# Kernel optimization log

Hardware: AMD Instinct MI355X
Metric: run time of the kernel (lower is better)

## Reference

```python
import jax, jax.numpy as jnp
import numpy as np

# --- fixed OpenCV filter kernels ---
# cv2.getGaussianKernel(3, 1): exp(-(i-1)^2/2), normalized -> [0.27407, 0.45186, 0.27407]
_g = np.exp(-((np.arange(3) - 1.0) ** 2) / 2.0)
GAUSS_1D = (_g / _g.sum()).astype(np.float32)
# cv2 Sobel/Laplacian ksize=9 separable parts (unnormalized, as cv2.Laplacian uses):
#   smoothing = binomial row C(8,k); second derivative = C(6,k) conv [1,-2,1]
SMOOTH_9 = np.array([1, 8, 28, 56, 70, 56, 28, 8, 1], dtype=np.float32)
D2_9 = np.array([1, 4, 4, -4, -10, -4, 4, 4, 1], dtype=np.float32)


def _depthwise_conv(x, k2d):
    """Depthwise 2D correlation with BORDER_REFLECT_101 padding (cv2 default).

    x: [N,H,W,C] float, k2d: [kh,kw] float (symmetric, so corr == conv)."""
    C = x.shape[-1]
    rh, rw = k2d.shape[0] // 2, k2d.shape[1] // 2
    # jnp 'reflect' == OpenCV BORDER_REFLECT_101 (edge pixel not duplicated)
    xp = jnp.pad(x, ((0, 0), (rh, rh), (rw, rw), (0, 0)), mode='reflect')
    k = jnp.broadcast_to(k2d[:, :, None, None], (k2d.shape[0], k2d.shape[1], 1, C))
    return jax.lax.conv_general_dilated(
        xp, k, window_strides=(1, 1), padding='VALID',
        dimension_numbers=('NHWC', 'HWIO', 'NHWC'),
        feature_group_count=C)


def setup_inputs() -> dict:
    key = jax.random.key(0)
    # uint8-range image batch, as the original layer feeds uint8 data to OpenCV
    x = jax.random.uniform(key, (32, 512, 512, 3), dtype=jnp.float32) * 255.0
    return {"x": x}


def reference(x) -> jnp.ndarray:
    g = jnp.asarray(GAUSS_1D)
    blur = _depthwise_conv(x, jnp.outer(g, g))  # GaussianBlur(ksize=3, sigma=1)
    lap_k = jnp.asarray(np.outer(SMOOTH_9, D2_9) + np.outer(D2_9, SMOOTH_9))
    lap = _depthwise_conv(blur, lap_k) + 1.0  # delta = 1
    # CV_8UC1 destination depth -> saturate to [0, 255]
    return jnp.clip(lap, 0.0, 255.0)
```

## Files before the change

kernel.cpp:

```cpp
#include <hip/hip_runtime.h>


#define TH 16
#define TW 32
#define FW (TW*3)
#define BP (TW+8)
#define BFU (BP*3)
#define BF 132
#define BHR (TH+8)
#define HIMG 512
#define WIMG 512
#define ROWF (WIMG*3)

__device__ __forceinline__ int reflect101(int i, int n) {
    i = (i < 0) ? -i : i;
    return (i >= n) ? (2 * n - 2 - i) : i;
}

__device__ __forceinline__ float4 fma4(float s, const float4& a, const float4& b) {
    return make_float4(fmaf(s, a.x, b.x), fmaf(s, a.y, b.y),
                       fmaf(s, a.z, b.z), fmaf(s, a.w, b.w));
}

__global__ __launch_bounds__(256, 5)
void log_fused(const float* __restrict__ x, float* __restrict__ out) {
    __shared__ __align__(16) float blur[BHR * BF];
    __shared__ __align__(16) float t1[TH * BF];
    __shared__ __align__(16) float t2[TH * BF];

    const int tid  = threadIdx.x;
    const int col0 = blockIdx.x * TW;
    const int row0 = blockIdx.y * TH;
    const float* const xn = x + (size_t)blockIdx.z * HIMG * ROWF;

    const float G0 = 0.2740686190f, G1 = 0.4518627620f;

    if (tid < 240) {
        const int lc = tid % BFU;
        const int rg = tid / BFU;
        const int p  = lc / 3;
        const int ch = lc - 3 * p;
        const int gc = reflect101(col0 - 4 + p, WIMG);
        const int xm = reflect101(gc - 1, WIMG) * 3 + ch;
        const int x0 = gc * 3 + ch;
        const int xp = reflect101(gc + 1, WIMG) * 3 + ch;
        #pragma unroll
        for (int r = rg; r < BHR; r += 2) {
            const int g  = row0 - 4 + r;
            const int gr = reflect101(g, HIMG);
            const float* pa = xn + (size_t)reflect101(gr - 1, HIMG) * ROWF;
            const float* pb = xn + (size_t)gr * ROWF;
            const float* pc = xn + (size_t)reflect101(gr + 1, HIMG) * ROWF;
            const float h0 = G0 * (pa[xm] + pa[xp]) + G1 * pa[x0];
            const float h1 = G0 * (pb[xm] + pb[xp]) + G1 * pb[x0];
            const float h2 = G0 * (pc[xm] + pc[xp]) + G1 * pc[x0];
            blur[r * BF + lc] = G0 * (h0 + h2) + G1 * h1;
        }
    }
    __syncthreads();

    const float S9[9] = {1.f, 8.f, 28.f, 56.f, 70.f, 56.f, 28.f, 8.f, 1.f};
    const float D9[9] = {1.f, 4.f, 4.f, -4.f, -10.f, -4.f, 4.f, 4.f, 1.f};

    if (tid < 240) {
        const int rg  = tid / 30;
        const int qc  = tid - rg * 30;
        const int lr0 = rg * 2;
        const int lc  = qc * 4;
        float4 w[10];
        #pragma unroll
        for (int k = 0; k < 10; ++k)
            w[k] = *(const float4*)&blur[(lr0 + k) * BF + lc];
        float4 a1r0 = make_float4(0.f, 0.f, 0.f, 0.f), a2r0 = a1r0;
        float4 a1r1 = a1r0, a2r1 = a1r0;
        #pragma unroll
        for (int k = 0; k < 9; ++k) {
            a1r0 = fma4(S9[k], w[k],     a1r0);
            a2r0 = fma4(D9[k], w[k],     a2r0);
            a1r1 = fma4(S9[k], w[k + 1], a1r1);
            a2r1 = fma4(D9[k], w[k + 1], a2r1);
        }
        *(float4*)&t1[(lr0    ) * BF + lc] = a1r0;
        *(float4*)&t1[(lr0 + 1) * BF + lc] = a1r1;
        *(float4*)&t2[(lr0    ) * BF + lc] = a2r0;
        *(float4*)&t2[(lr0 + 1) * BF + lc] = a2r1;
    }
    __syncthreads();

    if (tid < 192) {
        const int lr = tid / 12;
        const int qp = tid - lr * 12;
        const int lc = qp * 8;
        float w1[32], w2[32];
        #pragma unroll
        for (int q = 0; q < 8; ++q) {
            float4 v = *(const float4*)&t1[lr * BF + lc + 4 * q];
            w1[4*q+0] = v.x; w1[4*q+1] = v.y; w1[4*q+2] = v.z; w1[4*q+3] = v.w;
            float4 u = *(const float4*)&t2[lr * BF + lc + 4 * q];
            w2[4*q+0] = u.x; w2[4*q+1] = u.y; w2[4*q+2] = u.z; w2[4*q+3] = u.w;
        }
        float o[8];
        #pragma unroll
        for (int j = 0; j < 8; ++j) {
            float a = 1.0f;
            #pragma unroll
            for (int k = 0; k < 9; ++k) {
                a = fmaf(D9[k], w1[j + 3 * k], a);
                a = fmaf(S9[k], w2[j + 3 * k], a);
            }
            o[j] = fminf(fmaxf(a, 0.0f), 255.0f);
        }
        float* op = out + (size_t)blockIdx.z * HIMG * ROWF
                        + (size_t)(row0 + lr) * ROWF + (size_t)(col0 * 3 + lc);
        *(float4*)&op[0] = make_float4(o[0], o[1], o[2], o[3]);
        *(float4*)&op[4] = make_float4(o[4], o[5], o[6], o[7]);
    }
}

extern "C" void kernel_launch(void* const* d_in, const int* in_sizes, int n_in,
                              void* d_out, int out_size, void* d_ws, size_t ws_size,
                              hipStream_t stream) {
    const float* x = (const float*)d_in[0];
    float* outp = (float*)d_out;
    const int nimg = in_sizes[0] / (HIMG * WIMG * 3);
    dim3 grid(WIMG / TW, HIMG / TH, nimg);
    log_fused<<<grid, dim3(256, 1, 1), 0, stream>>>(x, outp);
}
```

Before: 264.4 us.

## Rewrite LoG as row-scan kernel with folded 11-tap filters and async LDS loads

```diff
diff --git a/kernel.cpp b/kernel.cpp
--- a/kernel.cpp
+++ b/kernel.cpp
@@ -1,119 +1,258 @@
 #include <hip/hip_runtime.h>
 
 
-#define TH 16
-#define TW 32
-#define FW (TW*3)
-#define BP (TW+8)
-#define BFU (BP*3)
-#define BF 132
-#define BHR (TH+8)
-#define HIMG 512
-#define WIMG 512
-#define ROWF (WIMG*3)
+#define NT    384
+#define HIMG  512
+#define ROWF  1536
+#define CH    3
+#define BUFF  (CH*ROWF)
 
 __device__ __forceinline__ int reflect101(int i, int n) {
     i = (i < 0) ? -i : i;
-    return (i >= n) ? (2 * n - 2 - i) : i;
-}
-
-__device__ __forceinline__ float4 fma4(float s, const float4& a, const float4& b) {
-    return make_float4(fmaf(s, a.x, b.x), fmaf(s, a.y, b.y),
-                       fmaf(s, a.z, b.z), fmaf(s, a.w, b.w));
-}
-
-__global__ __launch_bounds__(256, 5)
-void log_fused(const float* __restrict__ x, float* __restrict__ out) {
-    __shared__ __align__(16) float blur[BHR * BF];
-    __shared__ __align__(16) float t1[TH * BF];
-    __shared__ __align__(16) float t2[TH * BF];
-
-    const int tid  = threadIdx.x;
-    const int col0 = blockIdx.x * TW;
-    const int row0 = blockIdx.y * TH;
-    const float* const xn = x + (size_t)blockIdx.z * HIMG * ROWF;
-
-    const float G0 = 0.2740686190f, G1 = 0.4518627620f;
-
-    if (tid < 240) {
-        const int lc = tid % BFU;
-        const int rg = tid / BFU;
-        const int p  = lc / 3;
-        const int ch = lc - 3 * p;
-        const int gc = reflect101(col0 - 4 + p, WIMG);
-        const int xm = reflect101(gc - 1, WIMG) * 3 + ch;
-        const int x0 = gc * 3 + ch;
-        const int xp = reflect101(gc + 1, WIMG) * 3 + ch;
-        #pragma unroll
-        for (int r = rg; r < BHR; r += 2) {
-            const int g  = row0 - 4 + r;
-            const int gr = reflect101(g, HIMG);
-            const float* pa = xn + (size_t)reflect101(gr - 1, HIMG) * ROWF;
-            const float* pb = xn + (size_t)gr * ROWF;
-            const float* pc = xn + (size_t)reflect101(gr + 1, HIMG) * ROWF;
-            const float h0 = G0 * (pa[xm] + pa[xp]) + G1 * pa[x0];
-            const float h1 = G0 * (pb[xm] + pb[xp]) + G1 * pb[x0];
-            const float h2 = G0 * (pc[xm] + pc[xp]) + G1 * pc[x0];
-            blur[r * BF + lc] = G0 * (h0 + h2) + G1 * h1;
-        }
-    }
-    __syncthreads();
-
-    const float S9[9] = {1.f, 8.f, 28.f, 56.f, 70.f, 56.f, 28.f, 8.f, 1.f};
-    const float D9[9] = {1.f, 4.f, 4.f, -4.f, -10.f, -4.f, 4.f, 4.f, 1.f};
-
-    if (tid < 240) {
-        const int rg  = tid / 30;
-        const int qc  = tid - rg * 30;
-        const int lr0 = rg * 2;
-        const int lc  = qc * 4;
-        float4 w[10];
-        #pragma unroll
-        for (int k = 0; k < 10; ++k)
-            w[k] = *(const float4*)&blur[(lr0 + k) * BF + lc];
-        float4 a1r0 = make_float4(0.f, 0.f, 0.f, 0.f), a2r0 = a1r0;
-        float4 a1r1 = a1r0, a2r1 = a1r0;
-        #pragma unroll
-        for (int k = 0; k < 9; ++k) {
-            a1r0 = fma4(S9[k], w[k],     a1r0);
-            a2r0 = fma4(D9[k], w[k],     a2r0);
-            a1r1 = fma4(S9[k], w[k + 1], a1r1);
-            a2r1 = fma4(D9[k], w[k + 1], a2r1);
-        }
-        *(float4*)&t1[(lr0    ) * BF + lc] = a1r0;
-        *(float4*)&t1[(lr0 + 1) * BF + lc] = a1r1;
-        *(float4*)&t2[(lr0    ) * BF + lc] = a2r0;
-        *(float4*)&t2[(lr0 + 1) * BF + lc] = a2r1;
-    }
-    __syncthreads();
-
-    if (tid < 192) {
-        const int lr = tid / 12;
-        const int qp = tid - lr * 12;
-        const int lc = qp * 8;
-        float w1[32], w2[32];
-        #pragma unroll
-        for (int q = 0; q < 8; ++q) {
-            float4 v = *(const float4*)&t1[lr * BF + lc + 4 * q];
-            w1[4*q+0] = v.x; w1[4*q+1] = v.y; w1[4*q+2] = v.z; w1[4*q+3] = v.w;
-            float4 u = *(const float4*)&t2[lr * BF + lc + 4 * q];
-            w2[4*q+0] = u.x; w2[4*q+1] = u.y; w2[4*q+2] = u.z; w2[4*q+3] = u.w;
-        }
-        float o[8];
-        #pragma unroll
-        for (int j = 0; j < 8; ++j) {
-            float a = 1.0f;
+    return (i >= n) ? (2*n - 2 - i) : i;
+}
+
+__device__ constexpr float SGc[11] = {
+    0.27406861900052384f, 2.6444117140031430f, 11.562892047006810f,
+    30.192548952004191f, 52.163039333992666f, 62.326078667985332f,
+    52.163039333992666f, 30.192548952004191f, 11.562892047006810f,
+    2.6444117140031430f, 0.27406861900052384f};
+__device__ constexpr float DGc[11] = {
+    0.27406861900052384f, 1.5481372380010477f, 3.1777941429984285f,
+    1.8074510479958093f, -3.4518627619989523f, -6.7111765719937139f,
+    -3.4518627619989523f, 1.8074510479958093f, 3.1777941429984285f,
+    1.5481372380010477f, 0.27406861900052384f};
+
+__device__ __forceinline__ void gload1k(const float* g, float* l) {
+    __builtin_amdgcn_global_load_lds(
+        (const __attribute__((address_space(1))) void*)g,
+        (__attribute__((address_space(3))) void*)l, 16, 0, 0);
+}
+
+__device__ __forceinline__ void prefetch3(const float* g, float* l, int tid) {
+    const int wave = tid >> 6, lane = tid & 63;
+    const float* gp = g + wave*768 + lane*4;
+    float* lp = l + wave*768;
+    #pragma unroll
+    for (int i = 0; i < 3; ++i) gload1k(gp + i*256, lp + i*256);
+}
+
+__device__ __forceinline__ void prefetch5(const float* g, float* l, int tid) {
+    const int wave = tid >> 6, lane = tid & 63;
+    const float* gp = g + wave*1280 + lane*4;
+    float* lp = l + wave*1280;
+    #pragma unroll
+    for (int i = 0; i < 5; ++i) gload1k(gp + i*256, lp + i*256);
+}
+
+__device__ __forceinline__ void compute_h(const float* __restrict__ row, int cq,
+        const float* __restrict__ wSt, const float* __restrict__ wDt,
+        float4& hs, float4& hd) {
+    if (cq >= 4 && cq <= 379) {
+        float w[36];
+        const float4* wp = (const float4*)(row + 4*cq - 16);
+        #pragma unroll
+        for (int q = 0; q < 9; ++q) {
+            float4 v = wp[q];
+            w[4*q+0] = v.x; w[4*q+1] = v.y; w[4*q+2] = v.z; w[4*q+3] = v.w;
+        }
+        float hsv[4], hdv[4];
+        #pragma unroll
+        for (int j = 0; j < 4; ++j) {
+            float c = w[j+16];
+            float s = SGc[5]*c, d = DGc[5]*c;
             #pragma unroll
-            for (int k = 0; k < 9; ++k) {
-                a = fmaf(D9[k], w1[j + 3 * k], a);
-                a = fmaf(S9[k], w2[j + 3 * k], a);
-            }
-            o[j] = fminf(fmaxf(a, 0.0f), 255.0f);
-        }
-        float* op = out + (size_t)blockIdx.z * HIMG * ROWF
-                        + (size_t)(row0 + lr) * ROWF + (size_t)(col0 * 3 + lc);
-        *(float4*)&op[0] = make_float4(o[0], o[1], o[2], o[3]);
-        *(float4*)&op[4] = make_float4(o[4], o[5], o[6], o[7]);
+            for (int k = 0; k < 5; ++k) {
+                float p = w[j+1+3*k] + w[j+31-3*k];
+                s = fmaf(SGc[k], p, s);
+                d = fmaf(DGc[k], p, d);
+            }
+            hsv[j] = s; hdv[j] = d;
+        }
+        hs = make_float4(hsv[0],hsv[1],hsv[2],hsv[3]);
+        hd = make_float4(hdv[0],hdv[1],hdv[2],hdv[3]);
+    } else {
+        float hsv[4], hdv[4];
+        #pragma unroll
+        for (int j = 0; j < 4; ++j) {
+            const int fc = 4*cq + j;
+            const int pc = fc / 3;
+            const int ch = fc - 3*pc;
+            float s = 0.f, d = 0.f;
+            if (pc <= 4) {
+                #pragma unroll
+                for (int m = 0; m < 10; ++m) {
+                    float xv = row[3*m + ch];
+                    s = fmaf(wSt[pc*10+m], xv, s);
+                    d = fmaf(wDt[pc*10+m], xv, d);
+                }
+            } else if (pc >= 507) {
+                const int p = 511 - pc;
+                #pragma unroll
+                for (int m = 0; m < 10; ++m) {
+                    float xv = row[3*(511-m) + ch];
+                    s = fmaf(wSt[p*10+m], xv, s);
+                    d = fmaf(wDt[p*10+m], xv, d);
+                }
+            } else {
+                #pragma unroll
+                for (int k = 0; k < 11; ++k) {
+                    float xv = row[fc - 15 + 3*k];
+                    s = fmaf(SGc[k], xv, s);
+                    d = fmaf(DGc[k], xv, d);
+                }
+            }
+            hsv[j] = s; hdv[j] = d;
+        }
+        hs = make_float4(hsv[0],hsv[1],hsv[2],hsv[3]);
+        hd = make_float4(hdv[0],hdv[1],hdv[2],hdv[3]);
+    }
+}
+
+template<int S>
+__device__ __forceinline__ void do_step(const float* __restrict__ row, int cq,
+        const float* __restrict__ wSt, const float* __restrict__ wDt,
+        float4 (&acc)[12], bool fin, float* __restrict__ outq, int r_abs) {
+    float4 hs, hd;
+    compute_h(row, cq, wSt, wDt, hs, hd);
+    #pragma unroll
+    for (int k = 0; k <= 10; ++k) {
+        const int sl = (S - k + 24) % 12;
+        float4 a = acc[sl];
+        a.x = fmaf(SGc[k], hd.x, a.x); a.y = fmaf(SGc[k], hd.y, a.y);
+        a.z = fmaf(SGc[k], hd.z, a.z); a.w = fmaf(SGc[k], hd.w, a.w);
+        a.x = fmaf(DGc[k], hs.x, a.x); a.y = fmaf(DGc[k], hs.y, a.y);
+        a.z = fmaf(DGc[k], hs.z, a.z); a.w = fmaf(DGc[k], hs.w, a.w);
+        acc[sl] = a;
+    }
+    if (fin) {
+        const int fs = (S + 2) % 12;
+        float4 o = acc[fs];
+        o.x = fminf(fmaxf(o.x, 0.f), 255.f);
+        o.y = fminf(fmaxf(o.y, 0.f), 255.f);
+        o.z = fminf(fmaxf(o.z, 0.f), 255.f);
+        o.w = fminf(fmaxf(o.w, 0.f), 255.f);
+        *(float4*)(outq + (size_t)r_abs * ROWF) = o;
+        acc[fs] = make_float4(1.f,1.f,1.f,1.f);
+    }
+    acc[(S+1)%12] = make_float4(1.f,1.f,1.f,1.f);
+}
+
+__global__ __launch_bounds__(NT, 3)
+void log_scan(const float* __restrict__ x, float* __restrict__ out) {
+    __shared__ __align__(16) float smem[2*BUFF + 200];
+    float* buf0 = smem;
+    float* buf1 = smem + BUFF;
+    float* wSt  = smem + 2*BUFF;
+    float* wDt  = smem + 2*BUFF + 100;
+
+    const int tid = threadIdx.x;
+    const int img = blockIdx.y;
+    const float* xn = x   + (size_t)img * HIMG * ROWF;
+    float* on       = out + (size_t)img * HIMG * ROWF;
+    float* outq     = on + 4*tid;
+
+    if (tid < 100) {
+        const int f = tid / 50, rem = tid % 50, pc = rem / 10, m = rem % 10;
+        const double F9s[9] = {1,8,28,56,70,56,28,8,1};
+        const double F9d[9] = {1,4,4,-4,-10,-4,4,4,1};
+        const double A = 0.27406861900052384, B = 0.45186276199895232;
+        const double g3[3] = {A, B, A};
+        double acc = 0.0;
+        for (int j = 0; j < 9; ++j) {
+            int b = reflect101(pc - 4 + j, HIMG);
+            double fj = f ? F9d[j] : F9s[j];
+            for (int i = 0; i < 3; ++i)
+                if (reflect101(b - 1 + i, HIMG) == m) acc += fj * g3[i];
+        }
+        (f ? wDt : wSt)[pc*10 + m] = (float)acc;
+    }
+
+    if (blockIdx.x >= 2) {
+        const int band = blockIdx.x - 2;
+        const int r0 = (band == 15) ? 475 : (5 + 32*band);
+        const int g0 = r0 - 5;
+        prefetch3(xn + (size_t)g0*ROWF, buf0, tid);
+        float4 acc[12];
+        #pragma unroll
+        for (int i = 0; i < 12; ++i) acc[i] = make_float4(1.f,1.f,1.f,1.f);
+
+        for (int cc = 0; cc < 3; ++cc) {
+            const int c0 = 4*cc;
+            const int gb = 12*cc;
+            const bool fA = (cc > 0);
+            __syncthreads();
+            prefetch3(xn + (size_t)(g0 + CH*(c0+1))*ROWF, buf1, tid);
+            do_step<0>(buf0 + 0*ROWF, tid, wSt, wDt, acc, fA, outq, r0+gb-10);
+            do_step<1>(buf0 + 1*ROWF, tid, wSt, wDt, acc, fA, outq, r0+gb-9);
+            do_step<2>(buf0 + 2*ROWF, tid, wSt, wDt, acc, fA, outq, r0+gb-8);
+            __syncthreads();
+            prefetch3(xn + (size_t)(g0 + CH*(c0+2))*ROWF, buf0, tid);
+            do_step<3>(buf1 + 0*ROWF, tid, wSt, wDt, acc, fA, outq, r0+gb-7);
+            do_step<4>(buf1 + 1*ROWF, tid, wSt, wDt, acc, fA, outq, r0+gb-6);
+            do_step<5>(buf1 + 2*ROWF, tid, wSt, wDt, acc, fA, outq, r0+gb-5);
+            __syncthreads();
+            prefetch3(xn + (size_t)(g0 + CH*(c0+3))*ROWF, buf1, tid);
+            do_step<6>(buf0 + 0*ROWF, tid, wSt, wDt, acc, fA, outq, r0+gb-4);
+            do_step<7>(buf0 + 1*ROWF, tid, wSt, wDt, acc, fA, outq, r0+gb-3);
+            do_step<8>(buf0 + 2*ROWF, tid, wSt, wDt, acc, fA, outq, r0+gb-2);
+            __syncthreads();
+            prefetch3(xn + (size_t)(g0 + CH*(c0+4))*ROWF, buf0, tid);
+            do_step<9>(buf1 + 0*ROWF, tid, wSt, wDt, acc, fA, outq, r0+gb-1);
+            do_step<10>(buf1 + 1*ROWF, tid, wSt, wDt, acc, true, outq, r0+gb);
+            do_step<11>(buf1 + 2*ROWF, tid, wSt, wDt, acc, true, outq, r0+gb+1);
+        }
+        __syncthreads();
+        prefetch3(xn + (size_t)(g0 + CH*13)*ROWF, buf1, tid);
+        do_step<0>(buf0 + 0*ROWF, tid, wSt, wDt, acc, true, outq, r0+26);
+        do_step<1>(buf0 + 1*ROWF, tid, wSt, wDt, acc, true, outq, r0+27);
+        do_step<2>(buf0 + 2*ROWF, tid, wSt, wDt, acc, true, outq, r0+28);
+        __syncthreads();
+        do_step<3>(buf1 + 0*ROWF, tid, wSt, wDt, acc, true, outq, r0+29);
+        do_step<4>(buf1 + 1*ROWF, tid, wSt, wDt, acc, true, outq, r0+30);
+        do_step<5>(buf1 + 2*ROWF, tid, wSt, wDt, acc, true, outq, r0+31);
+    } else {
+        const int top = (blockIdx.x == 0);
+        const int base = top ? 0 : (HIMG - 10);
+        prefetch5(xn + (size_t)base*ROWF, smem, tid);
+        float4 accB[5];
+        #pragma unroll
+        for (int r = 0; r < 5; ++r) accB[r] = make_float4(1.f,1.f,1.f,1.f);
+
+        #pragma unroll
+        for (int half = 0; half < 2; ++half) {
+            __syncthreads();
+            for (int q = 0; q < 5; ++q) {
+                float4 hs, hd;
+                compute_h(smem + q*ROWF, tid, wSt, wDt, hs, hd);
+                const int qq = half*5 + q;
+                const int m = top ? qq : (9 - qq);
+                #pragma unroll
+                for (int r = 0; r < 5; ++r) {
+                    float ws = wSt[r*10+m], wd = wDt[r*10+m];
+                    float4 a = accB[r];
+                    a.x = fmaf(ws, hd.x, a.x); a.y = fmaf(ws, hd.y, a.y);
+                    a.z = fmaf(ws, hd.z, a.z); a.w = fmaf(ws, hd.w, a.w);
+                    a.x = fmaf(wd, hs.x, a.x); a.y = fmaf(wd, hs.y, a.y);
+                    a.z = fmaf(wd, hs.z, a.z); a.w = fmaf(wd, hs.w, a.w);
+                    accB[r] = a;
+                }
+            }
+            if (half == 0) {
+                __syncthreads();
+                prefetch5(xn + (size_t)(base+5)*ROWF, smem, tid);
+            }
+        }
+        #pragma unroll
+        for (int r = 0; r < 5; ++r) {
+            const int r_abs = top ? r : (511 - r);
+            float4 o = accB[r];
+            o.x = fminf(fmaxf(o.x, 0.f), 255.f);
+            o.y = fminf(fmaxf(o.y, 0.f), 255.f);
+            o.z = fminf(fmaxf(o.z, 0.f), 255.f);
+            o.w = fminf(fmaxf(o.w, 0.f), 255.f);
+            *(float4*)(on + (size_t)r_abs*ROWF + 4*tid) = o;
+        }
     }
 }
 
@@ -122,7 +261,7 @@
                               hipStream_t stream) {
     const float* x = (const float*)d_in[0];
     float* outp = (float*)d_out;
-    const int nimg = in_sizes[0] / (HIMG * WIMG * 3);
-    dim3 grid(WIMG / TW, HIMG / TH, nimg);
-    log_fused<<<grid, dim3(256, 1, 1), 0, stream>>>(x, outp);
-}
+    const int nimg = in_sizes[0] / (HIMG * ROWF);
+    dim3 grid(18, nimg, 1);
+    log_scan<<<grid, dim3(NT, 1, 1), 0, stream>>>(x, outp);
+}
```

Measured after the change: 541.7 us. 2.05x slower.
